# Kernel optimization log

Measured on AMD Instinct MI355X. Metric: run time of the kernel, lower is better.

## Reference

```python
import jax, jax.numpy as jnp
import numpy as np

WS = 8            # window size (square)
HEADS = 16
HEAD_DIM = 32
DIM = 512
NEG_INF = float('-inf')


def _create_mask(ws, disp, upper_lower, left_right):
    size = ws * ws
    m = np.zeros((size, size), dtype=np.float32)
    d = disp
    if upper_lower:
        m[-d * ws:, :-d * ws] = NEG_INF
        m[:-d * ws, -d * ws:] = NEG_INF
    if left_right:
        m = m.reshape(ws, ws, ws, ws)
        m[:, -d:, :, :-d] = NEG_INF
        m[:, :-d, :, -d:] = NEG_INF
        m = m.reshape(size, size)
    return m


def _relative_indices(ws):
    coords = np.array([[x, y] for x in range(ws) for y in range(ws)])  # [ws^2, 2]
    dist = coords[None, :, :] - coords[:, None, :]                      # [ws^2, ws^2, 2]
    dist += ws - 1
    return dist.astype(np.int64)


_REL_IDX = _relative_indices(WS)                      # [64, 64, 2]
_UL_MASK = jnp.asarray(_create_mask(WS, WS // 2, True, False))   # [64, 64]
_LR_MASK = jnp.asarray(_create_mask(WS, WS // 2, False, True))   # [64, 64]


def setup_inputs() -> dict:
    key = jax.random.key(0)
    ks = jax.random.split(key, 5)
    b, n = 16, 64
    return {
        'x': jax.random.normal(ks[0], (b, n, n, DIM), dtype=jnp.float32),
        'w_qkv': jax.random.normal(ks[1], (3 * HEADS * HEAD_DIM, DIM), dtype=jnp.float32) * 0.02,
        'pos_embedding': jax.random.normal(ks[2], (2 * WS - 1, 2 * WS - 1), dtype=jnp.float32),
        'w_out': jax.random.normal(ks[3], (DIM, HEADS * HEAD_DIM), dtype=jnp.float32) * 0.02,
        'b_out': jax.random.normal(ks[4], (DIM,), dtype=jnp.float32) * 0.02,
    }


def reference(x, w_qkv, pos_embedding, w_out, b_out):
    disp = WS // 2
    scale = HEAD_DIM ** -0.5
    b, n_h, n_w, _ = x.shape
    nw_h, nw_w = n_h // WS, n_w // WS

    # cyclic shift (shifted=True)
    x = jnp.roll(x, shift=(-disp, -disp), axis=(1, 2))

    qkv = x @ w_qkv.T                                   # [b, n_h, n_w, 3*h*d]
    qkv = qkv.reshape(b, nw_h, WS, nw_w, WS, 3, HEADS, HEAD_DIM)
    # -> [3, b, heads, n_windows, window_tokens, head_dim]
    qkv = qkv.transpose(5, 0, 6, 1, 3, 2, 4, 7).reshape(
        3, b, HEADS, nw_h * nw_w, WS * WS, HEAD_DIM)
    q, k, v = qkv[0], qkv[1], qkv[2]

    dots = jnp.einsum('bhwid,bhwjd->bhwij', q, k) * scale
    # relative position bias
    dots = dots + pos_embedding[_REL_IDX[:, :, 0], _REL_IDX[:, :, 1]]
    # shift masks: last window-row and last window-column
    dots = dots.at[:, :, -nw_w:].add(_UL_MASK)
    dots = dots.at[:, :, nw_w - 1::nw_w].add(_LR_MASK)

    attn = jax.nn.softmax(dots, axis=-1)
    out = jnp.einsum('bhwij,bhwjd->bhwid', attn, v)     # [b,h,nw,ws^2,d]

    out = out.reshape(b, HEADS, nw_h, nw_w, WS, WS, HEAD_DIM)
    out = out.transpose(0, 2, 4, 3, 5, 1, 6).reshape(b, n_h, n_w, HEADS * HEAD_DIM)
    out = out @ w_out.T + b_out

    out = jnp.roll(out, shift=(disp, disp), axis=(1, 2))
    return out
```

## Files before the change

### kernel.cpp

```cpp
#include <hip/hip_runtime.h>
#include <hip/hip_bf16.h>
#include <stdint.h>

typedef __bf16 bf16;
typedef __attribute__((ext_vector_type(4))) float f32x4;
typedef __attribute__((ext_vector_type(8))) bf16 bf16x8;
typedef __attribute__((ext_vector_type(4))) bf16 bf16x4;

#define AS1 __attribute__((address_space(1)))
#define AS3 __attribute__((address_space(3)))

static __device__ __forceinline__ void gload_lds16(const bf16* g, bf16* l) {
  __builtin_amdgcn_global_load_lds((const AS1 void*)g, (AS3 void*)l, 16, 0, 0);
}

#define BAR __builtin_amdgcn_s_barrier()
#define SCHED0 __builtin_amdgcn_sched_barrier(0)
#define VMC_(n) asm volatile("s_waitcnt vmcnt(" #n ")" ::: "memory")
#define VMC(n) VMC_(n)
#define LGKM0 asm volatile("s_waitcnt lgkmcnt(0)" ::: "memory")

#define STAGE_A(gsrc, dst, kt_) do {                                          \
  _Pragma("unroll") for (int s_ = 0; s_ < 4; ++s_) {                          \
    int idx_ = s_ * 256 + tid;                                                \
    int r_ = idx_ >> 3, c_ = idx_ & 7;                                        \
    gload_lds16((gsrc) + (size_t)r_ * 512 + ((kt_) << 6) + ((c_ ^ (r_ & 7)) << 3), \
                (dst) + idx_ * 8);                                            \
  }                                                                           \
} while (0)

#define LOADB(ktq, NCOLX) do {                                                \
  const bf16* bp_ = Bptr + (size_t)(ktq) * ((size_t)(NCOLX) * 64);            \
  _Pragma("unroll") for (int cb_ = 0; cb_ < 4; ++cb_)                         \
  _Pragma("unroll") for (int ks_ = 0; ks_ < 2; ++ks_)                         \
    bfr[cb_][ks_] = *(const bf16x8*)(bp_ + cb_ * 128 + (size_t)ks_ * (NCOLX) * 32); \
} while (0)

#define KLOOP_BD(Ag, NCOLX)                                                   \
  f32x4 acc[4][4] = {};                                                       \
  bf16x8 af[4][2], bfr[4][2];                                                 \
  STAGE_A(Ag, SA0, 0);                                                        \
  LOADB(0, NCOLX);                                                            \
  VMC(8); BAR;                                                                \
  STAGE_A(Ag, SA1, 1);                                                        \
  _Pragma("unroll 2")                                                         \
  for (int kt = 0; kt < 8; ++kt) {                                            \
    bf16* Ap = (kt & 1) ? SA1 : SA0;                                          \
    _Pragma("unroll") for (int i_ = 0; i_ < 4; ++i_) {                        \
      int ra_ = wr + i_ * 16 + lr;                                            \
      _Pragma("unroll") for (int ks_ = 0; ks_ < 2; ++ks_)                     \
        af[i_][ks_] = *(const bf16x8*)(Ap + ra_ * 64 + (((ks_ * 4 + lg) ^ (ra_ & 7)) << 3)); \
    }                                                                         \
    LGKM0; SCHED0;                                                            \
    __builtin_amdgcn_s_setprio(1);                                            \
    _Pragma("unroll") for (int i_ = 0; i_ < 4; ++i_)                          \
    _Pragma("unroll") for (int j_ = 0; j_ < 4; ++j_)                          \
    _Pragma("unroll") for (int ks_ = 0; ks_ < 2; ++ks_)                       \
      acc[i_][j_] = __builtin_amdgcn_mfma_f32_16x16x32_bf16(                  \
          af[i_][ks_], bfr[j_][ks_], acc[i_][j_], 0, 0, 0);                   \
    __builtin_amdgcn_s_setprio(0);                                            \
    if (kt < 7) LOADB(kt + 1, NCOLX);                                         \
    if (kt < 7) { VMC(8); }                                                   \
    BAR;                                                                      \
    if (kt < 6) STAGE_A(Ag, Ap, kt + 2);                                      \
  }

__global__ __launch_bounds__(256) void prep_all(
    const float* __restrict__ x, const float* __restrict__ wqkv,
    const float* __restrict__ wout, const float* __restrict__ pos,
    bf16* __restrict__ xst, bf16* __restrict__ wqkv_bt,
    bf16* __restrict__ wout_bt, float* __restrict__ bias4) {
  const int blk = blockIdx.x, tid = threadIdx.x;
  if (blk < 1024) {
    int m = blk * 64 + (tid & 63);
    int w = tid >> 6;
    int b = m >> 12, win = (m >> 6) & 63, t = m & 63;
    int ip = ((win >> 3) << 3) + (t >> 3);
    int jp = ((win & 7) << 3) + (t & 7);
    int io = (ip + 4) & 63, jo = (jp + 4) & 63;
    const float* src = x + ((((size_t)(b << 6) + io) << 6) + jo) * 512;
    bf16* dst = xst + (size_t)m * 8;
    #pragma unroll
    for (int it = 0; it < 4; ++it) {
      int kb0 = w * 16 + it * 4;
      float4 v[8];
      #pragma unroll
      for (int q = 0; q < 8; ++q) v[q] = *(const float4*)(src + kb0 * 8 + q * 4);
      #pragma unroll
      for (int c = 0; c < 4; ++c) {
        bf16x8 o = { (bf16)v[2*c].x, (bf16)v[2*c].y, (bf16)v[2*c].z, (bf16)v[2*c].w,
                     (bf16)v[2*c+1].x, (bf16)v[2*c+1].y, (bf16)v[2*c+1].z, (bf16)v[2*c+1].w };
        *(bf16x8*)(dst + (size_t)(kb0 + c) * 524288) = o;
      }
    }
  } else if (blk < 1280) {
    int r = (blk - 1024) * 8 + (tid >> 5);
    int lane = tid & 31;
    if (r < 1536) {
      int part = r >> 9, h = (r >> 5) & 15, d = r & 31;
      int col = part * 32 + d;
      float sc = (part == 0) ? 0.17677669529663689f : 1.0f;
      const float* src = wqkv + (size_t)r * 512;
      #pragma unroll
      for (int kb = lane; kb < 64; kb += 32) {
        int kt = kb >> 3, ch = kb & 7;
        float4 v0 = *(const float4*)(src + kb * 8);
        float4 v1 = *(const float4*)(src + kb * 8 + 4);
        bf16x8 o = { (bf16)(v0.x * sc), (bf16)(v0.y * sc), (bf16)(v0.z * sc), (bf16)(v0.w * sc),
                     (bf16)(v1.x * sc), (bf16)(v1.y * sc), (bf16)(v1.z * sc), (bf16)(v1.w * sc) };
        *(bf16x8*)(wqkv_bt + (size_t)(h * 8 + kt) * 6144 + col * 64 + ((ch ^ (col & 7)) << 3)) = o;
      }
    } else {
      int r2 = r - 1536;
      const float* src = wout + (size_t)r2 * 512;
      #pragma unroll
      for (int kb = lane; kb < 64; kb += 32) {
        float4 v0 = *(const float4*)(src + kb * 8);
        float4 v1 = *(const float4*)(src + kb * 8 + 4);
        bf16x8 o = { (bf16)v0.x, (bf16)v0.y, (bf16)v0.z, (bf16)v0.w,
                     (bf16)v1.x, (bf16)v1.y, (bf16)v1.z, (bf16)v1.w };
        *(bf16x8*)(wout_bt + ((size_t)kb * 512 + r2) * 8) = o;
      }
    }
  } else {
    int idx = (blk - 1280) * 256 + tid;
    int ty = idx >> 12, ij = idx & 4095;
    int i = ij >> 6, j = ij & 63;
    int rx = ((j >> 3) - (i >> 3)) + 7;
    int ry = ((j & 7) - (i & 7)) + 7;
    float v = pos[rx * 15 + ry];
    if ((ty & 1) && (((i ^ j) >> 5) & 1)) v = -1e30f;
    if ((ty & 2) && (((i ^ j) >> 2) & 1)) v = -1e30f;
    bias4[idx] = v;
  }
}

#define LOADAF(dst, ktq) do {                                                 \
  _Pragma("unroll") for (int i_ = 0; i_ < 2; ++i_)                            \
  _Pragma("unroll") for (int ks_ = 0; ks_ < 2; ++ks_)                         \
    dst[i_][ks_] = *(const bf16x8*)(Aptr + ((size_t)((ktq) * 8 + ks_ * 4 + lg)) * 524288 + i_ * 128); \
} while (0)

#define STAGE_B(dstbuf, ktq) do {                                             \
  const bf16* src_ = Bh + (size_t)(ktq) * 6144;                               \
  _Pragma("unroll") for (int s_ = 0; s_ < 3; ++s_) {                          \
    int idx_ = s_ * 256 + tid;                                                \
    gload_lds16(src_ + idx_ * 8, (dstbuf) + idx_ * 8);                        \
  }                                                                           \
} while (0)

#define KTB(CUR, NXT, KT_) do {                                               \
  const bf16* Bp_ = smb + ((KT_) & 1) * 6144;                                 \
  _Pragma("unroll") for (int cb_ = 0; cb_ < 6; ++cb_)                         \
  _Pragma("unroll") for (int ks_ = 0; ks_ < 2; ++ks_) {                       \
    int col_ = cb_ * 16 + lr;                                                 \
    bfr[cb_][ks_] = *(const bf16x8*)(Bp_ + col_ * 64 + (((ks_ * 4 + lg) ^ (col_ & 7)) << 3)); \
  }                                                                           \
  if ((KT_) < 7) LOADAF(NXT, (KT_) + 1);                                      \
  if ((KT_) < 7) { VMC(7); } else { VMC(0); }                                 \
  LGKM0; SCHED0;                                                              \
  __builtin_amdgcn_s_setprio(1);                                              \
  _Pragma("unroll") for (int i_ = 0; i_ < 2; ++i_)                            \
  _Pragma("unroll") for (int j_ = 0; j_ < 6; ++j_)                            \
  _Pragma("unroll") for (int ks_ = 0; ks_ < 2; ++ks_)                         \
    acc[i_][j_] = __builtin_amdgcn_mfma_f32_16x16x32_bf16(                    \
        CUR[i_][ks_], bfr[j_][ks_], acc[i_][j_], 0, 0, 0);                    \
  __builtin_amdgcn_s_setprio(0);                                              \
  if ((KT_) < 7) { VMC(4); }                                                  \
  BAR;                                                                        \
  if ((KT_) < 6) STAGE_B(smb + ((KT_) & 1) * 6144, (KT_) + 2);                \
} while (0)

__global__ __launch_bounds__(256, 3) void qkv_attn(
    const bf16* __restrict__ xst, const bf16* __restrict__ wb2,
    const float* __restrict__ bias4, bf16* __restrict__ ao) {
  __shared__ bf16 smb[12288];

  const int tid = threadIdx.x, wave = tid >> 6, lane = tid & 63;
  const int ww = wave >> 1, rh = wave & 1;
  const int lr = lane & 15, lg = lane >> 4;

  int bid = blockIdx.x;
  bid = (bid & 7) * 1024 + (bid >> 3);
  const int mt = bid >> 4, h = bid & 15;

  const bf16* Aptr = xst + ((size_t)(mt * 128 + ww * 64 + rh * 32 + lr)) * 8;
  const bf16* Bh = wb2 + (size_t)h * 49152;

  f32x4 acc[2][6] = {};
  bf16x8 afA[2][2], afB[2][2], bfr[6][2];

  STAGE_B(smb, 0);
  LOADAF(afA, 0);
  VMC(4); BAR;
  STAGE_B(smb + 6144, 1);

  KTB(afA, afB, 0);
  KTB(afB, afA, 1);
  KTB(afA, afB, 2);
  KTB(afB, afA, 3);
  KTB(afA, afB, 4);
  KTB(afB, afA, 5);
  KTB(afA, afB, 6);
  KTB(afB, afA, 7);

  bf16* Eu = smb + ww * 6144;
  bf16* Ev = Eu + 4096;
  #pragma unroll
  for (int i = 0; i < 2; ++i)
    #pragma unroll
    for (int r = 0; r < 4; ++r) {
      int row = rh * 32 + i * 16 + (lg << 2) + r;
      #pragma unroll
      for (int j = 0; j < 4; ++j) {
        int c = j * 16 + lr;
        Eu[row * 64 + (c ^ ((row & 7) << 3))] = (bf16)acc[i][j][r];
      }
      #pragma unroll
      for (int j = 4; j < 6; ++j) {
        int cv = (j - 4) * 16 + lr;
        Ev[cv * 64 + (row ^ ((cv & 7) << 3))] = (bf16)acc[i][j][r];
      }
    }
  LGKM0; BAR;

  bf16x8 qf[2], kf[4];
  #pragma unroll
  for (int i = 0; i < 2; ++i) {
    int ra = rh * 32 + i * 16 + lr;
    qf[i] = *(const bf16x8*)(Eu + ra * 64 + ((lg << 3) ^ ((ra & 7) << 3)));
  }
  #pragma unroll
  for (int j = 0; j < 4; ++j) {
    int rb = j * 16 + lr;
    kf[j] = *(const bf16x8*)(Eu + rb * 64 + ((32 + (lg << 3)) ^ ((rb & 7) << 3)));
  }
  f32x4 s[2][4] = {};
  #pragma unroll
  for (int i = 0; i < 2; ++i)
    #pragma unroll
    for (int j = 0; j < 4; ++j)
      s[i][j] = __builtin_amdgcn_mfma_f32_16x16x32_bf16(qf[i], kf[j], s[i][j], 0, 0, 0);

  const int gw = mt * 2 + ww;
  const int win = gw & 63;
  const int ty = ((win >= 56) ? 1 : 0) | (((win & 7) == 7) ? 2 : 0);
  const float* bt = bias4 + ty * 4096;
  #pragma unroll
  for (int i = 0; i < 2; ++i)
    #pragma unroll
    for (int r = 0; r < 4; ++r) {
      int grow = rh * 32 + i * 16 + (lg << 2) + r;
      #pragma unroll
      for (int j = 0; j < 4; ++j)
        s[i][j][r] += bt[grow * 64 + j * 16 + lr];
    }
  #pragma unroll
  for (int i = 0; i < 2; ++i)
    #pragma unroll
    for (int r = 0; r < 4; ++r) {
      float mx = fmaxf(fmaxf(s[i][0][r], s[i][1][r]), fmaxf(s[i][2][r], s[i][3][r]));
      mx = fmaxf(mx, __shfl_xor(mx, 1));
      mx = fmaxf(mx, __shfl_xor(mx, 2));
      mx = fmaxf(mx, __shfl_xor(mx, 4));
      mx = fmaxf(mx, __shfl_xor(mx, 8));
      float sum = 0.f;
      #pragma unroll
      for (int j = 0; j < 4; ++j) { s[i][j][r] = __expf(s[i][j][r] - mx); sum += s[i][j][r]; }
      sum += __shfl_xor(sum, 1);
      sum += __shfl_xor(sum, 2);
      sum += __shfl_xor(sum, 4);
      sum += __shfl_xor(sum, 8);
      float inv = 1.0f / sum;
      #pragma unroll
      for (int j = 0; j < 4; ++j) s[i][j][r] *= inv;
    }
  BAR;
  #pragma unroll
  for (int i = 0; i < 2; ++i)
    #pragma unroll
    for (int r = 0; r < 4; ++r) {
      int row = rh * 32 + i * 16 + (lg << 2) + r;
      #pragma unroll
      for (int j = 0; j < 4; ++j) {
        int c = j * 16 + lr;
        Eu[row * 64 + (c ^ ((row & 7) << 3))] = (bf16)s[i][j][r];
      }
    }
  LGKM0; SCHED0;
  bf16x8 vf[2][2];
  #pragma unroll
  for (int kk = 0; kk < 2; ++kk)
    #pragma unroll
    for (int nj = 0; nj < 2; ++nj) {
      int dv = nj * 16 + lr;
      vf[kk][nj] = *(const bf16x8*)(Ev + dv * 64 + ((kk * 32 + (lg << 3)) ^ ((dv & 7) << 3)));
    }
  f32x4 o[2][2] = {};
  #pragma unroll
  for (int kk = 0; kk < 2; ++kk)
    #pragma unroll
    for (int mi = 0; mi < 2; ++mi) {
      int ra = rh * 32 + mi * 16 + lr;
      bf16x8 pa = *(const bf16x8*)(Eu + ra * 64 + ((kk * 32 + (lg << 3)) ^ ((ra & 7) << 3)));
      #pragma unroll
      for (int nj = 0; nj < 2; ++nj)
        o[mi][nj] = __builtin_amdgcn_mfma_f32_16x16x32_bf16(pa, vf[kk][nj], o[mi][nj], 0, 0, 0);
    }
  bf16* dst = ao + ((size_t)(mt * 128 + ww * 64)) * 512 + h * 32;
  #pragma unroll
  for (int mi = 0; mi < 2; ++mi)
    #pragma unroll
    for (int r = 0; r < 4; ++r) {
      int t = rh * 32 + mi * 16 + (lg << 2) + r;
      #pragma unroll
      for (int nj = 0; nj < 2; ++nj)
        dst[(size_t)t * 512 + nj * 16 + lr] = (bf16)o[mi][nj][r];
    }
}

__global__ __launch_bounds__(256, 3) void gemm_out(
    const bf16* __restrict__ ao, const bf16* __restrict__ wob,
    const float* __restrict__ bout, float* __restrict__ out) {
  __shared__ bf16 SA[2][8192];
  bf16* SA0 = SA[0]; bf16* SA1 = SA[1];

  const int tid = threadIdx.x, wave = tid >> 6, lane = tid & 63;
  int bid = blockIdx.x;
  bid = (bid & 7) * 256 + (bid >> 3);
  const int mt = bid >> 2, nt = bid & 3;
  const bf16* Ag = ao + ((size_t)mt * 128) * 512;
  const int wr = (wave >> 1) << 6, wc = (wave & 1) << 6;
  const int lr = lane & 15, lg = lane >> 4;
  const bf16* Bptr = wob + (((size_t)lg * 512) + nt * 128 + wc + lr) * 8;

  KLOOP_BD(Ag, 512)

  float bv[4];
  #pragma unroll
  for (int j = 0; j < 4; ++j) bv[j] = bout[nt * 128 + wc + j * 16 + lr];
  #pragma unroll
  for (int i = 0; i < 4; ++i)
    #pragma unroll
    for (int r = 0; r < 4; ++r) {
      int m = (mt << 7) + wr + i * 16 + (lg << 2) + r;
      int b = m >> 12, win = (m >> 6) & 63, t = m & 63;
      int ip = ((win >> 3) << 3) + (t >> 3);
      int jp = ((win & 7) << 3) + (t & 7);
      int io = (ip + 4) & 63, jo = (jp + 4) & 63;
      float* orow = out + ((((size_t)(b << 6) + io) << 6) + jo) * 512 + nt * 128 + wc;
      #pragma unroll
      for (int j = 0; j < 4; ++j)
        orow[j * 16 + lr] = acc[i][j][r] + bv[j];
    }
}

extern "C" void kernel_launch(void* const* d_in, const int* in_sizes, int n_in,
                              void* d_out, int out_size, void* d_ws, size_t ws_size,
                              hipStream_t stream) {
  const float* x    = (const float*)d_in[0];
  const float* wqkv = (const float*)d_in[1];
  const float* pos  = (const float*)d_in[2];
  const float* wout = (const float*)d_in[3];
  const float* bout = (const float*)d_in[4];
  float* out = (float*)d_out;

  char* ws = (char*)d_ws;
  bf16* xst     = (bf16*)(ws);
  bf16* ao      = (bf16*)(ws + 67108864);
  bf16* wqkv_bt = (bf16*)(ws + 268435456);
  bf16* wout_bt = (bf16*)(ws + 270008320);
  float* bias4  = (float*)(ws + 270532608);

  prep_all<<<dim3(1344), dim3(256), 0, stream>>>(x, wqkv, wout, pos,
                                                 xst, wqkv_bt, wout_bt, bias4);
  qkv_attn<<<dim3(8192), dim3(256), 0, stream>>>(xst, wqkv_bt, bias4, ao);
  gemm_out<<<dim3(2048), dim3(256), 0, stream>>>(ao, wout_bt, bout, out);
}
```

Measured before the change: 246.8 us.

## Double qkv_attn block to 512 threads covering four windows with paired B staging

The fused QKV+attention kernel now uses 512-thread blocks that each process four windows (256 tokens) for one head instead of two. Each weight slice staged into LDS is therefore shared by twice as many waves, and the weight staging is restructured to load two k-steps per stage with a barrier every two k-steps instead of every step. This aims to halve redundant weight loads and reduce barrier frequency, at the cost of doubled LDS per block, coarser pipelining with fewer overlap points, and fewer blocks in flight.

New measurement: 385.7 us. 56.3% more time.

```diff
diff --git a/kernel.cpp b/kernel.cpp
--- a/kernel.cpp
+++ b/kernel.cpp
@@ -141,24 +141,23 @@
     dst[i_][ks_] = *(const bf16x8*)(Aptr + ((size_t)((ktq) * 8 + ks_ * 4 + lg)) * 524288 + i_ * 128); \
 } while (0)
 
-#define STAGE_B(dstbuf, ktq) do {                                             \
-  const bf16* src_ = Bh + (size_t)(ktq) * 6144;                               \
+#define PSTAGE(dstbuf, pr) do {                                               \
+  const bf16* src_ = Bh + (size_t)(pr) * 12288;                               \
   _Pragma("unroll") for (int s_ = 0; s_ < 3; ++s_) {                          \
-    int idx_ = s_ * 256 + tid;                                                \
+    int idx_ = s_ * 512 + tid;                                                \
     gload_lds16(src_ + idx_ * 8, (dstbuf) + idx_ * 8);                        \
   }                                                                           \
 } while (0)
 
-#define KTB(CUR, NXT, KT_) do {                                               \
-  const bf16* Bp_ = smb + ((KT_) & 1) * 6144;                                 \
+#define KTB(CUR, NXT, KT_, VN) do {                                           \
+  const bf16* Bp_ = smb + ((((KT_) >> 1) & 1) * 12288) + (((KT_) & 1) * 6144); \
   _Pragma("unroll") for (int cb_ = 0; cb_ < 6; ++cb_)                         \
   _Pragma("unroll") for (int ks_ = 0; ks_ < 2; ++ks_) {                       \
     int col_ = cb_ * 16 + lr;                                                 \
     bfr[cb_][ks_] = *(const bf16x8*)(Bp_ + col_ * 64 + (((ks_ * 4 + lg) ^ (col_ & 7)) << 3)); \
   }                                                                           \
   if ((KT_) < 7) LOADAF(NXT, (KT_) + 1);                                      \
-  if ((KT_) < 7) { VMC(7); } else { VMC(0); }                                 \
-  LGKM0; SCHED0;                                                              \
+  VMC(VN); LGKM0; SCHED0;                                                     \
   __builtin_amdgcn_s_setprio(1);                                              \
   _Pragma("unroll") for (int i_ = 0; i_ < 2; ++i_)                            \
   _Pragma("unroll") for (int j_ = 0; j_ < 6; ++j_)                            \
@@ -166,43 +165,40 @@
     acc[i_][j_] = __builtin_amdgcn_mfma_f32_16x16x32_bf16(                    \
         CUR[i_][ks_], bfr[j_][ks_], acc[i_][j_], 0, 0, 0);                    \
   __builtin_amdgcn_s_setprio(0);                                              \
-  if ((KT_) < 7) { VMC(4); }                                                  \
-  BAR;                                                                        \
-  if ((KT_) < 6) STAGE_B(smb + ((KT_) & 1) * 6144, (KT_) + 2);                \
-} while (0)
-
-__global__ __launch_bounds__(256, 3) void qkv_attn(
+} while (0)
+
+__global__ __launch_bounds__(512, 4) void qkv_attn(
     const bf16* __restrict__ xst, const bf16* __restrict__ wb2,
     const float* __restrict__ bias4, bf16* __restrict__ ao) {
-  __shared__ bf16 smb[12288];
+  __shared__ bf16 smb[24576];
 
   const int tid = threadIdx.x, wave = tid >> 6, lane = tid & 63;
   const int ww = wave >> 1, rh = wave & 1;
   const int lr = lane & 15, lg = lane >> 4;
 
   int bid = blockIdx.x;
-  bid = (bid & 7) * 1024 + (bid >> 3);
+  bid = (bid & 7) * 512 + (bid >> 3);
   const int mt = bid >> 4, h = bid & 15;
 
-  const bf16* Aptr = xst + ((size_t)(mt * 128 + ww * 64 + rh * 32 + lr)) * 8;
+  const bf16* Aptr = xst + ((size_t)(mt * 256 + ww * 64 + rh * 32 + lr)) * 8;
   const bf16* Bh = wb2 + (size_t)h * 49152;
 
   f32x4 acc[2][6] = {};
   bf16x8 afA[2][2], afB[2][2], bfr[6][2];
 
-  STAGE_B(smb, 0);
+  PSTAGE(smb, 0);
   LOADAF(afA, 0);
-  VMC(4); BAR;
-  STAGE_B(smb + 6144, 1);
-
-  KTB(afA, afB, 0);
-  KTB(afB, afA, 1);
-  KTB(afA, afB, 2);
-  KTB(afB, afA, 3);
-  KTB(afA, afB, 4);
-  KTB(afB, afA, 5);
-  KTB(afA, afB, 6);
-  KTB(afB, afA, 7);
+  PSTAGE(smb + 12288, 1);
+  VMC(7); BAR;
+
+  KTB(afA, afB, 0, 7);
+  KTB(afB, afA, 1, 4); BAR; PSTAGE(smb, 2);
+  KTB(afA, afB, 2, 7);
+  KTB(afB, afA, 3, 4); BAR; PSTAGE(smb + 12288, 3);
+  KTB(afA, afB, 4, 7);
+  KTB(afB, afA, 5, 4); BAR;
+  KTB(afA, afB, 6, 4);
+  KTB(afB, afA, 7, 0); BAR;
 
   bf16* Eu = smb + ww * 6144;
   bf16* Ev = Eu + 4096;
@@ -242,7 +238,7 @@
     for (int j = 0; j < 4; ++j)
       s[i][j] = __builtin_amdgcn_mfma_f32_16x16x32_bf16(qf[i], kf[j], s[i][j], 0, 0, 0);
 
-  const int gw = mt * 2 + ww;
+  const int gw = mt * 4 + ww;
   const int win = gw & 63;
   const int ty = ((win >= 56) ? 1 : 0) | (((win & 7) == 7) ? 2 : 0);
   const float* bt = bias4 + ty * 4096;
@@ -307,7 +303,7 @@
       for (int nj = 0; nj < 2; ++nj)
         o[mi][nj] = __builtin_amdgcn_mfma_f32_16x16x32_bf16(pa, vf[kk][nj], o[mi][nj], 0, 0, 0);
     }
-  bf16* dst = ao + ((size_t)(mt * 128 + ww * 64)) * 512 + h * 32;
+  bf16* dst = ao + ((size_t)(mt * 256 + ww * 64)) * 512 + h * 32;
   #pragma unroll
   for (int mi = 0; mi < 2; ++mi)
     #pragma unroll
@@ -374,6 +370,6 @@
 
   prep_all<<<dim3(1344), dim3(256), 0, stream>>>(x, wqkv, wout, pos,
                                                  xst, wqkv_bt, wout_bt, bias4);
-  qkv_attn<<<dim3(8192), dim3(256), 0, stream>>>(xst, wqkv_bt, bias4, ao);
+  qkv_attn<<<dim3(4096), dim3(512), 0, stream>>>(xst, wqkv_bt, bias4, ao);
   gemm_out<<<dim3(2048), dim3(256), 0, stream>>>(ao, wout_bt, bout, out);
 }
```
